# Performance work log

Measured on AMD Instinct MI355X. Metric: run time of the kernel, lower is better.

Reference implementation:

```python
import jax, jax.numpy as jnp
import numpy as np

B, L, H = 32, 512, 1024
H2 = H // 2          # split half = 512
D_ATTN = 64
EPS = 1e-5


def setup_inputs() -> dict:
    key = jax.random.key(0)
    ks = jax.random.split(key, 6)
    x = jax.random.normal(ks[0], (B, L, H), dtype=jnp.float32)
    # LayerNorm params (default torch init: weight=1, bias=0)
    ln_gamma = jnp.ones((H2,), jnp.float32)
    ln_beta = jnp.zeros((H2,), jnp.float32)
    # Toeplitz params (module inits w_vector=0, bias=1; use small random w for nontrivial math)
    w_vector = jax.random.normal(ks[1], (2 * L - 1,), jnp.float32) * 0.02
    t_bias = jnp.ones((L,), jnp.float32)
    # TinyAttention: kqv Linear(H2 -> 3*d_attn), proj Linear(d_attn -> H2)
    kqv_w = jax.random.normal(ks[2], (H2, 3 * D_ATTN), jnp.float32) * 0.02
    kqv_b = jnp.zeros((3 * D_ATTN,), jnp.float32)
    proj_w = jax.random.normal(ks[3], (D_ATTN, H2), jnp.float32) * 0.02
    proj_b = jnp.zeros((H2,), jnp.float32)
    return {"x": x, "ln_gamma": ln_gamma, "ln_beta": ln_beta,
            "w_vector": w_vector, "t_bias": t_bias,
            "kqv_w": kqv_w, "kqv_b": kqv_b, "proj_w": proj_w, "proj_b": proj_b}


def _toeplitz(w_vector):
    # Faithful replication of get_toeplitz(): pad, tile, trim, reshape, crop.
    r = w_vector.shape[0] // 2            # = L - 1
    t = jnp.pad(w_vector, (0, L))         # length 3L - 1
    t = jnp.tile(t, L)[:-L]               # length L * (3L - 2)
    t = t.reshape(L, 3 * L - 2)
    return t[:, r:-r]                      # [L, L]


def _tiny_attention(v, kqv_w, kqv_b, proj_w, proj_b):
    kqv = v @ kqv_w + kqv_b                        # [B, L, 3*d_attn]
    k, q, val = jnp.split(kqv, 3, axis=-1)         # chunk order: key, query, value
    scale = 1.0 / jnp.sqrt(jnp.float32(q.shape[-1]))
    scores = jnp.einsum('bqd,bkd->bqk', q, k) * scale
    soft = jax.nn.softmax(scores, axis=-1)
    head = jnp.einsum('bqk,bkd->bqd', soft, val)   # [B, L, d_attn]
    return head @ proj_w + proj_b                  # [B, L, H2]


def reference(x, ln_gamma, ln_beta, w_vector, t_bias, kqv_w, kqv_b, proj_w, proj_b):
    u, v = jnp.split(x, 2, axis=-1)                # each [B, L, H2]
    head = _tiny_attention(v, kqv_w, kqv_b, proj_w, proj_b)
    # LayerNorm over last dim
    mu = jnp.mean(v, axis=-1, keepdims=True)
    var = jnp.mean(jnp.square(v - mu), axis=-1, keepdims=True)
    vn = (v - mu) * jax.lax.rsqrt(var + EPS) * ln_gamma + ln_beta
    # spatial (Toeplitz) mixing: permute -> [B, H2, L], matmul [L, L], bias
    w_t = _toeplitz(w_vector)
    vm = jnp.einsum('blc,lm->bmc', vn, w_t.T).transpose(0, 2, 1)  # keep faithful: vp @ w_t
    vm = jnp.einsum('bcl,lm->bcm', vn.transpose(0, 2, 1), w_t) + t_bias
    v_out = vm.transpose(0, 2, 1) + head           # [B, L, H2]
    return u * v_out
```

## Files before the change

kernel.cpp:

```cpp
#include <hip/hip_runtime.h>
#include <math.h>

#define NB 32
#define LL 512
#define HH 1024
#define H2 512
#define DA 64

typedef unsigned int u32;
typedef unsigned short u16;
typedef __bf16 bf16x8 __attribute__((ext_vector_type(8)));
typedef float f32x4 __attribute__((ext_vector_type(4)));

__device__ __forceinline__ u16 f2bu(float f) {
    u32 u = __builtin_bit_cast(u32, f);
    u = (u + 0x7fff + ((u >> 16) & 1)) >> 16;
    return (u16)u;
}

__device__ __forceinline__ float b2f(u16 u) {
    u32 v = (u32)u << 16;
    return __builtin_bit_cast(float, v);
}

__device__ __forceinline__ void async_cp16(const void* g, void* l) {
    __builtin_amdgcn_global_load_lds(
        (const __attribute__((address_space(1))) u32*)g,
        (__attribute__((address_space(3))) u32*)l, 16, 0, 0);
}

__global__ void prep_kernel(const float* __restrict__ wv,
                            const float* __restrict__ kqvw,
                            const float* __restrict__ projw,
                            u16* __restrict__ wt, u16* __restrict__ kqvwT,
                            u16* __restrict__ projwT) {
    int e = blockIdx.x * 256 + threadIdx.x;
    if (e < 262144) {
        int m = e >> 9, l = e & 511;
        wt[e] = f2bu(wv[511 + m - l]);
    } else if (e < 262144 + 98304) {
        int i = e - 262144;
        int n = i >> 9, k = i & 511;
        kqvwT[i] = f2bu(kqvw[(size_t)k * 192 + n]);
    } else {
        int i = e - 360448;
        int c = i >> 6, d = i & 63;
        projwT[i] = f2bu(projw[(size_t)d * 512 + c]);
    }
}

__global__ __launch_bounds__(256, 2)
void front_kernel(const float* __restrict__ x,
                  const float* __restrict__ gamma, const float* __restrict__ beta,
                  const u16* __restrict__ kqvwT, const float* __restrict__ kqvb,
                  u16* __restrict__ vnT,
                  u16* __restrict__ qb, u16* __restrict__ kb, u16* __restrict__ vT) {
    __shared__ u16 Bs[2][192 * 32];
    __shared__ u16 T[512 * 34];
    __shared__ float MUs[32], RSs[32];
    int blk = blockIdx.x, t = threadIdx.x;
    int b = blk >> 4, l0 = (blk & 15) * 32;
    int lane = t & 63, wid = t >> 6;
    int l15 = lane & 15, q16 = lane >> 4, q8 = q16 * 8;

#pragma unroll
    for (int s = 0; s < 3; ++s) {
        int ci = t + s * 256;
        int grow = ci >> 2, gcol = ((ci & 3) ^ (grow & 3)) << 3;
        async_cp16(kqvwT + (size_t)grow * 512 + gcol, &Bs[0][ci * 8]);
    }

    int r = t >> 3, q = t & 7;
    const float* xr = x + ((size_t)(b * LL + l0 + r)) * HH + H2;
    float s1 = 0.0f, s2 = 0.0f;
#pragma unroll
    for (int i = 0; i < 16; ++i) {
        float4 v = *(const float4*)(xr + q * 64 + i * 4);
        s1 += v.x + v.y + v.z + v.w;
        s2 += v.x * v.x + v.y * v.y + v.z * v.z + v.w * v.w;
        int c = q * 64 + i * 4;
        T[(c + 0) * 34 + r] = f2bu(v.x);
        T[(c + 1) * 34 + r] = f2bu(v.y);
        T[(c + 2) * 34 + r] = f2bu(v.z);
        T[(c + 3) * 34 + r] = f2bu(v.w);
    }
    s1 += __shfl_xor(s1, 1); s2 += __shfl_xor(s2, 1);
    s1 += __shfl_xor(s1, 2); s2 += __shfl_xor(s2, 2);
    s1 += __shfl_xor(s1, 4); s2 += __shfl_xor(s2, 4);
    float mu = s1 * (1.0f / H2);
    float rstd = rsqrtf(s2 * (1.0f / H2) - mu * mu + 1e-5f);
    if ((t & 7) == 0) { MUs[r] = mu; RSs[r] = rstd; }
    __syncthreads();

    {
        int cc = t >> 2, seg = t & 3;
        float m0 = MUs[seg * 8 + 0], r0s = RSs[seg * 8 + 0];
        float m1 = MUs[seg * 8 + 1], r1s = RSs[seg * 8 + 1];
        float m2 = MUs[seg * 8 + 2], r2s = RSs[seg * 8 + 2];
        float m3 = MUs[seg * 8 + 3], r3s = RSs[seg * 8 + 3];
        float m4 = MUs[seg * 8 + 4], r4s = RSs[seg * 8 + 4];
        float m5 = MUs[seg * 8 + 5], r5s = RSs[seg * 8 + 5];
        float m6 = MUs[seg * 8 + 6], r6s = RSs[seg * 8 + 6];
        float m7 = MUs[seg * 8 + 7], r7s = RSs[seg * 8 + 7];
#pragma unroll
        for (int pass = 0; pass < 8; ++pass) {
            int c = pass * 64 + cc;
            float ga = gamma[c], be = beta[c];
            const u16* Tp = T + c * 34 + seg * 8;
            ushort4 t0 = ((const ushort4*)Tp)[0];
            ushort4 t1 = ((const ushort4*)Tp)[1];
            ushort4 o0, o1;
            o0.x = f2bu((b2f(t0.x) - m0) * r0s * ga + be);
            o0.y = f2bu((b2f(t0.y) - m1) * r1s * ga + be);
            o0.z = f2bu((b2f(t0.z) - m2) * r2s * ga + be);
            o0.w = f2bu((b2f(t0.w) - m3) * r3s * ga + be);
            o1.x = f2bu((b2f(t1.x) - m4) * r4s * ga + be);
            o1.y = f2bu((b2f(t1.y) - m5) * r5s * ga + be);
            o1.z = f2bu((b2f(t1.z) - m6) * r6s * ga + be);
            o1.w = f2bu((b2f(t1.w) - m7) * r7s * ga + be);
            u16* dst = vnT + ((size_t)(b * H2 + c)) * LL + l0 + seg * 8;
            ((ushort4*)dst)[0] = o0;
            ((ushort4*)dst)[1] = o1;
        }
    }

    int wm = (wid & 1) * 16, wn = (wid >> 1) * 96;
    int rowA = wm + l15;
    f32x4 acc[6] = {};
    for (int it = 0; it < 16; ++it) {
        if (it < 15) {
            int k0n = (it + 1) * 32, bfn = (it + 1) & 1;
#pragma unroll
            for (int s = 0; s < 3; ++s) {
                int ci = t + s * 256;
                int grow = ci >> 2, gcol = ((ci & 3) ^ (grow & 3)) << 3;
                async_cp16(kqvwT + (size_t)grow * 512 + k0n + gcol, &Bs[bfn][ci * 8]);
            }
        }
        bf16x8 a;
        int kb0 = it * 32 + q8;
#pragma unroll
        for (int u = 0; u < 8; ++u)
            a[u] = __builtin_bit_cast(__bf16, T[(kb0 + u) * 34 + rowA]);
        const u16* Bp = &Bs[it & 1][0];
#pragma unroll
        for (int j = 0; j < 6; ++j) {
            int n = wn + j * 16 + l15;
            bf16x8 bb = *(const bf16x8*)(Bp + (n * 4 + (q16 ^ (n & 3))) * 8);
            acc[j] = __builtin_amdgcn_mfma_f32_16x16x32_bf16(a, bb, acc[j], 0, 0, 0);
        }
        __syncthreads();
    }

    u16* Ts = &Bs[0][0];
    int rq = q16 * 4;
#pragma unroll
    for (int rr = 0; rr < 4; ++rr) {
        int mloc = wm + rq + rr;
        size_t mg = (size_t)(b * LL + l0 + mloc);
#pragma unroll
        for (int j = 0; j < 6; ++j) {
            int n = wn + j * 16 + l15;
            u16 hv = f2bu(acc[j][rr] + kqvb[n]);
            if (n < 64)       kb[mg * 64 + n] = hv;
            else if (n < 128) qb[mg * 64 + (n - 64)] = hv;
            else              Ts[(n - 128) * 36 + mloc] = hv;
        }
    }
    __syncthreads();
    int d = t >> 2, lo2 = (t & 3) * 8;
    u16* dst = vT + ((size_t)(b * 64 + d)) * 512 + l0 + lo2;
    const u16* src = Ts + d * 36 + lo2;
    ((ushort4*)dst)[0] = ((const ushort4*)src)[0];
    ((ushort4*)dst)[1] = ((const ushort4*)src)[1];
}

#define VLD 136
__global__ __launch_bounds__(256, 4)
void attn_kernel(const u16* __restrict__ qb, const u16* __restrict__ kb,
                 const u16* __restrict__ vT, u16* __restrict__ head) {
    __shared__ u16 Ps[4 * 16 * VLD];
    __shared__ float Osh[4][16 * 65];
    __shared__ float Msh[4][16], Lsh[4][16];
    int b = blockIdx.y, q0 = blockIdx.x * 16;
    int t = threadIdx.x, lane = t & 63, w = t >> 6;
    int l15 = lane & 15, q16 = lane >> 4, q8 = q16 * 8;
    int kc = w * 128;
    const u16* qg = qb + (size_t)b * LL * DA;
    const u16* kg = kb + (size_t)b * LL * DA;
    const u16* vg = vT + (size_t)b * DA * LL;

    bf16x8 aq[2];
#pragma unroll
    for (int s = 0; s < 2; ++s)
        aq[s] = *(const bf16x8*)(qg + (size_t)(q0 + l15) * DA + s * 32 + q8);

    f32x4 sc[8] = {};
#pragma unroll
    for (int j = 0; j < 8; ++j) {
#pragma unroll
        for (int s = 0; s < 2; ++s) {
            bf16x8 bk = *(const bf16x8*)(kg + (size_t)(kc + j * 16 + l15) * DA + s * 32 + q8);
            sc[j] = __builtin_amdgcn_mfma_f32_16x16x32_bf16(aq[s], bk, sc[j], 0, 0, 0);
        }
    }
    float mx[4], sm[4];
#pragma unroll
    for (int j = 0; j < 8; ++j)
#pragma unroll
        for (int rr = 0; rr < 4; ++rr) sc[j][rr] *= 0.125f;
#pragma unroll
    for (int rr = 0; rr < 4; ++rr) {
        float m0 = sc[0][rr];
#pragma unroll
        for (int j = 1; j < 8; ++j) m0 = fmaxf(m0, sc[j][rr]);
        m0 = fmaxf(m0, __shfl_xor(m0, 1));
        m0 = fmaxf(m0, __shfl_xor(m0, 2));
        m0 = fmaxf(m0, __shfl_xor(m0, 4));
        m0 = fmaxf(m0, __shfl_xor(m0, 8));
        mx[rr] = m0;
    }
#pragma unroll
    for (int j = 0; j < 8; ++j)
#pragma unroll
        for (int rr = 0; rr < 4; ++rr) sc[j][rr] = __expf(sc[j][rr] - mx[rr]);
#pragma unroll
    for (int rr = 0; rr < 4; ++rr) {
        float s0 = sc[0][rr];
#pragma unroll
        for (int j = 1; j < 8; ++j) s0 += sc[j][rr];
        s0 += __shfl_xor(s0, 1);
        s0 += __shfl_xor(s0, 2);
        s0 += __shfl_xor(s0, 4);
        s0 += __shfl_xor(s0, 8);
        sm[rr] = s0;
    }
    u16* Pw = Ps + w * 16 * VLD;
#pragma unroll
    for (int j = 0; j < 8; ++j)
#pragma unroll
        for (int rr = 0; rr < 4; ++rr)
            Pw[(q16 * 4 + rr) * VLD + j * 16 + l15] = f2bu(sc[j][rr]);
    f32x4 o[4] = {};
#pragma unroll
    for (int kt = 0; kt < 4; ++kt) {
        bf16x8 ap = *(const bf16x8*)(Pw + l15 * VLD + kt * 32 + q8);
#pragma unroll
        for (int j = 0; j < 4; ++j) {
            bf16x8 bv = *(const bf16x8*)(vg + (size_t)(j * 16 + l15) * LL + kc + kt * 32 + q8);
            o[j] = __builtin_amdgcn_mfma_f32_16x16x32_bf16(ap, bv, o[j], 0, 0, 0);
        }
    }
#pragma unroll
    for (int j = 0; j < 4; ++j)
#pragma unroll
        for (int rr = 0; rr < 4; ++rr)
            Osh[w][(q16 * 4 + rr) * 65 + j * 16 + l15] = o[j][rr];
    if (l15 == 0) {
#pragma unroll
        for (int rr = 0; rr < 4; ++rr) {
            Msh[w][q16 * 4 + rr] = mx[rr];
            Lsh[w][q16 * 4 + rr] = sm[rr];
        }
    }
    __syncthreads();
    int qq = t >> 4, dg = (t & 15) * 4;
    float m0 = Msh[0][qq], m1 = Msh[1][qq], m2 = Msh[2][qq], m3 = Msh[3][qq];
    float ms = fmaxf(fmaxf(m0, m1), fmaxf(m2, m3));
    float f0 = __expf(m0 - ms), f1 = __expf(m1 - ms), f2 = __expf(m2 - ms), f3 = __expf(m3 - ms);
    float lst = Lsh[0][qq] * f0 + Lsh[1][qq] * f1 + Lsh[2][qq] * f2 + Lsh[3][qq] * f3;
    float inv = 1.0f / lst;
    ushort4 res;
    u16* rp = (u16*)&res;
#pragma unroll
    for (int i = 0; i < 4; ++i) {
        int idx = qq * 65 + dg + i;
        float a = Osh[0][idx] * f0 + Osh[1][idx] * f1 + Osh[2][idx] * f2 + Osh[3][idx] * f3;
        rp[i] = f2bu(a * inv);
    }
    *(ushort4*)(head + (size_t)(b * LL + q0 + qq) * DA + dg) = res;
}

__device__ __forceinline__ void mfma_tile64(const u16* As, const u16* Bs,
                                            f32x4 acc[4][4], int wm, int wn,
                                            int l15, int q16) {
    int s7 = l15 & 7;
#pragma unroll
    for (int kk = 0; kk < 2; ++kk) {
        int j0 = kk * 4 + q16;
        bf16x8 a[4], bv[4];
#pragma unroll
        for (int i = 0; i < 4; ++i) {
            int row = wm + i * 16 + l15;
            a[i] = *(const bf16x8*)(As + (row * 8 + (j0 ^ s7)) * 8);
        }
#pragma unroll
        for (int j = 0; j < 4; ++j) {
            int row = wn + j * 16 + l15;
            bv[j] = *(const bf16x8*)(Bs + (row * 8 + (j0 ^ s7)) * 8);
        }
#pragma unroll
        for (int i = 0; i < 4; ++i)
#pragma unroll
            for (int j = 0; j < 4; ++j)
                acc[i][j] = __builtin_amdgcn_mfma_f32_16x16x32_bf16(a[i], bv[j], acc[i][j], 0, 0, 0);
    }
}

__device__ __forceinline__ void stage_pair(const u16* A, const u16* B, int ldk,
                                           int koff, u16* Ad, u16* Bd, int t) {
#pragma unroll
    for (int s = 0; s < 4; ++s) {
        int ci = t + s * 256;
        int grow = ci >> 3, gcol = ((ci & 7) ^ (grow & 7)) << 3;
        async_cp16(A + (size_t)grow * ldk + koff + gcol, Ad + ci * 8);
        async_cp16(B + (size_t)grow * ldk + koff + gcol, Bd + ci * 8);
    }
}

__global__ __launch_bounds__(256, 2)
void mix_kernel(const u16* __restrict__ wt,
                const u16* __restrict__ vnT,
                const u16* __restrict__ headb,
                const u16* __restrict__ projwT,
                const float* __restrict__ x,
                const float* __restrict__ tbias,
                const float* __restrict__ projb,
                float* __restrict__ out) {
    __shared__ u16 As[2][128 * 64];
    __shared__ u16 Bs[2][128 * 64];
    int lid = blockIdx.x;
    int p8 = lid & 7, rest = lid >> 3;
    int mi = rest & 3, pair = (rest >> 2) * 8 + p8;
    int b = pair >> 2, m0 = mi * 128, c0 = (pair & 3) * 128;
    int t = threadIdx.x, lane = t & 63, wid = t >> 6;
    int wm = (wid >> 1) * 64, wn = (wid & 1) * 64;
    int l15 = lane & 15, q16 = lane >> 4;
    f32x4 acc[4][4] = {};
    const u16* Ag = wt + (size_t)m0 * 512;
    const u16* Bg = vnT + ((size_t)b * H2 + c0) * 512;
    const u16* Hg = headb + ((size_t)b * LL + m0) * DA;
    const u16* Pg = projwT + (size_t)c0 * DA;

    stage_pair(Ag, Bg, 512, 0, As[0], Bs[0], t);
    __syncthreads();

    for (int it = 0; it < 9; ++it) {
        int nx = it + 1;
        if (nx < 8)
            stage_pair(Ag, Bg, 512, nx * 64, As[nx & 1], Bs[nx & 1], t);
        else if (nx == 8)
            stage_pair(Hg, Pg, 64, 0, As[0], Bs[0], t);
        mfma_tile64(As[it & 1], Bs[it & 1], acc, wm, wn, l15, q16);
        __syncthreads();
    }

    int rq = q16 * 4;
#pragma unroll
    for (int i = 0; i < 4; ++i) {
#pragma unroll
        for (int rr = 0; rr < 4; ++rr) {
            int m = m0 + wm + i * 16 + rq + rr;
            float tb = tbias[m];
            const float* xrow = x + ((size_t)b * LL + m) * HH;
            float* orow = out + ((size_t)b * LL + m) * H2;
#pragma unroll
            for (int j = 0; j < 4; ++j) {
                int c = c0 + wn + j * 16 + l15;
                float val = acc[i][j][rr] + tb + projb[c];
                orow[c] = xrow[c] * val;
            }
        }
    }
}

extern "C" void kernel_launch(void* const* d_in, const int* in_sizes, int n_in,
                              void* d_out, int out_size, void* d_ws, size_t ws_size,
                              hipStream_t stream) {
    (void)in_sizes; (void)n_in; (void)out_size; (void)ws_size;
    const float* x     = (const float*)d_in[0];
    const float* gamma = (const float*)d_in[1];
    const float* beta  = (const float*)d_in[2];
    const float* wv    = (const float*)d_in[3];
    const float* tb    = (const float*)d_in[4];
    const float* kqvw  = (const float*)d_in[5];
    const float* kqvb  = (const float*)d_in[6];
    const float* projw = (const float*)d_in[7];
    const float* projb = (const float*)d_in[8];
    float* out = (float*)d_out;

    u16* vnT_bf  = (u16*)d_ws;
    u16* qb      = vnT_bf + (size_t)NB * LL * H2;
    u16* kb      = qb + (size_t)NB * LL * DA;
    u16* vTb     = kb + (size_t)NB * LL * DA;
    u16* head_bf = vTb + (size_t)NB * LL * DA;
    u16* wt_bf   = head_bf + (size_t)NB * LL * DA;
    u16* kqvwT   = wt_bf + 512 * 512;
    u16* projwT  = kqvwT + 192 * 512;

    prep_kernel <<<1536, 256, 0, stream>>>(wv, kqvw, projw, wt_bf, kqvwT, projwT);
    front_kernel<<<512, 256, 0, stream>>>(x, gamma, beta, kqvwT, kqvb,
                                          vnT_bf, qb, kb, vTb);
    attn_kernel <<<dim3(32, NB), 256, 0, stream>>>(qb, kb, vTb, head_bf);
    mix_kernel  <<<512, 256, 0, stream>>>(wt_bf, vnT_bf, head_bf, projwT,
                                          x, tb, projb, out);
}
```

Baseline: 173.5 us.

## Precompute LayerNorm stats in prep kernel and shrink front kernel tiles

```diff
diff --git a/kernel.cpp b/kernel.cpp
--- a/kernel.cpp
+++ b/kernel.cpp
@@ -32,147 +32,137 @@
 __global__ void prep_kernel(const float* __restrict__ wv,
                             const float* __restrict__ kqvw,
                             const float* __restrict__ projw,
+                            const float* __restrict__ x,
                             u16* __restrict__ wt, u16* __restrict__ kqvwT,
-                            u16* __restrict__ projwT) {
-    int e = blockIdx.x * 256 + threadIdx.x;
-    if (e < 262144) {
-        int m = e >> 9, l = e & 511;
-        wt[e] = f2bu(wv[511 + m - l]);
-    } else if (e < 262144 + 98304) {
-        int i = e - 262144;
-        int n = i >> 9, k = i & 511;
-        kqvwT[i] = f2bu(kqvw[(size_t)k * 192 + n]);
+                            u16* __restrict__ projwT, float2* __restrict__ stats) {
+    int blk = blockIdx.x, t = threadIdx.x;
+    if (blk < 1536) {
+        int e = blk * 256 + t;
+        if (e < 262144) {
+            int m = e >> 9, l = e & 511;
+            wt[e] = f2bu(wv[511 + m - l]);
+        } else if (e < 262144 + 98304) {
+            int i = e - 262144;
+            int n = i >> 9, k = i & 511;
+            kqvwT[i] = f2bu(kqvw[(size_t)k * 192 + n]);
+        } else {
+            int i = e - 360448;
+            int c = i >> 6, d = i & 63;
+            projwT[i] = f2bu(projw[(size_t)d * 512 + c]);
+        }
     } else {
-        int i = e - 360448;
-        int c = i >> 6, d = i & 63;
-        projwT[i] = f2bu(projw[(size_t)d * 512 + c]);
-    }
-}
-
-__global__ __launch_bounds__(256, 2)
+        int row = (blk - 1536) * 4 + (t >> 6);
+        int lane = t & 63;
+        const float* xr = x + (size_t)row * HH + H2;
+        float4 a = *(const float4*)(xr + lane * 4);
+        float4 c = *(const float4*)(xr + 256 + lane * 4);
+        float s1 = a.x + a.y + a.z + a.w + c.x + c.y + c.z + c.w;
+        float s2 = a.x*a.x + a.y*a.y + a.z*a.z + a.w*a.w
+                 + c.x*c.x + c.y*c.y + c.z*c.z + c.w*c.w;
+        s1 += __shfl_xor(s1, 1);  s2 += __shfl_xor(s2, 1);
+        s1 += __shfl_xor(s1, 2);  s2 += __shfl_xor(s2, 2);
+        s1 += __shfl_xor(s1, 4);  s2 += __shfl_xor(s2, 4);
+        s1 += __shfl_xor(s1, 8);  s2 += __shfl_xor(s2, 8);
+        s1 += __shfl_xor(s1, 16); s2 += __shfl_xor(s2, 16);
+        s1 += __shfl_xor(s1, 32); s2 += __shfl_xor(s2, 32);
+        if (lane == 0) {
+            float mu = s1 * (1.0f / H2);
+            float rstd = rsqrtf(s2 * (1.0f / H2) - mu * mu + 1e-5f);
+            stats[row] = make_float2(mu, rstd);
+        }
+    }
+}
+
+__global__ __launch_bounds__(256, 4)
 void front_kernel(const float* __restrict__ x,
                   const float* __restrict__ gamma, const float* __restrict__ beta,
+                  const float2* __restrict__ stats,
                   const u16* __restrict__ kqvwT, const float* __restrict__ kqvb,
                   u16* __restrict__ vnT,
                   u16* __restrict__ qb, u16* __restrict__ kb, u16* __restrict__ vT) {
-    __shared__ u16 Bs[2][192 * 32];
-    __shared__ u16 T[512 * 34];
-    __shared__ float MUs[32], RSs[32];
+    __shared__ u16 T[512 * 18];
     int blk = blockIdx.x, t = threadIdx.x;
-    int b = blk >> 4, l0 = (blk & 15) * 32;
+    int b = blk >> 5, l0 = (blk & 31) * 16;
     int lane = t & 63, wid = t >> 6;
     int l15 = lane & 15, q16 = lane >> 4, q8 = q16 * 8;
 
-#pragma unroll
-    for (int s = 0; s < 3; ++s) {
-        int ci = t + s * 256;
-        int grow = ci >> 2, gcol = ((ci & 3) ^ (grow & 3)) << 3;
-        async_cp16(kqvwT + (size_t)grow * 512 + gcol, &Bs[0][ci * 8]);
-    }
-
-    int r = t >> 3, q = t & 7;
-    const float* xr = x + ((size_t)(b * LL + l0 + r)) * HH + H2;
-    float s1 = 0.0f, s2 = 0.0f;
-#pragma unroll
-    for (int i = 0; i < 16; ++i) {
-        float4 v = *(const float4*)(xr + q * 64 + i * 4);
-        s1 += v.x + v.y + v.z + v.w;
-        s2 += v.x * v.x + v.y * v.y + v.z * v.z + v.w * v.w;
-        int c = q * 64 + i * 4;
-        T[(c + 0) * 34 + r] = f2bu(v.x);
-        T[(c + 1) * 34 + r] = f2bu(v.y);
-        T[(c + 2) * 34 + r] = f2bu(v.z);
-        T[(c + 3) * 34 + r] = f2bu(v.w);
-    }
-    s1 += __shfl_xor(s1, 1); s2 += __shfl_xor(s2, 1);
-    s1 += __shfl_xor(s1, 2); s2 += __shfl_xor(s2, 2);
-    s1 += __shfl_xor(s1, 4); s2 += __shfl_xor(s2, 4);
-    float mu = s1 * (1.0f / H2);
-    float rstd = rsqrtf(s2 * (1.0f / H2) - mu * mu + 1e-5f);
-    if ((t & 7) == 0) { MUs[r] = mu; RSs[r] = rstd; }
-    __syncthreads();
-
     {
-        int cc = t >> 2, seg = t & 3;
-        float m0 = MUs[seg * 8 + 0], r0s = RSs[seg * 8 + 0];
-        float m1 = MUs[seg * 8 + 1], r1s = RSs[seg * 8 + 1];
-        float m2 = MUs[seg * 8 + 2], r2s = RSs[seg * 8 + 2];
-        float m3 = MUs[seg * 8 + 3], r3s = RSs[seg * 8 + 3];
-        float m4 = MUs[seg * 8 + 4], r4s = RSs[seg * 8 + 4];
-        float m5 = MUs[seg * 8 + 5], r5s = RSs[seg * 8 + 5];
-        float m6 = MUs[seg * 8 + 6], r6s = RSs[seg * 8 + 6];
-        float m7 = MUs[seg * 8 + 7], r7s = RSs[seg * 8 + 7];
-#pragma unroll
-        for (int pass = 0; pass < 8; ++pass) {
-            int c = pass * 64 + cc;
-            float ga = gamma[c], be = beta[c];
-            const u16* Tp = T + c * 34 + seg * 8;
+        int r = t >> 4;
+        int c00 = (t & 15) * 4;
+        float2 st = stats[(size_t)(b * LL + l0 + r)];
+        const float* xr = x + ((size_t)(b * LL + l0 + r)) * HH + H2;
+#pragma unroll
+        for (int i = 0; i < 8; ++i) {
+            int c = c00 + i * 64;
+            float4 v = *(const float4*)(xr + c);
+            float4 g = *(const float4*)(gamma + c);
+            float4 be = *(const float4*)(beta + c);
+            T[(c + 0) * 18 + r] = f2bu((v.x - st.x) * st.y * g.x + be.x);
+            T[(c + 1) * 18 + r] = f2bu((v.y - st.x) * st.y * g.y + be.y);
+            T[(c + 2) * 18 + r] = f2bu((v.z - st.x) * st.y * g.z + be.z);
+            T[(c + 3) * 18 + r] = f2bu((v.w - st.x) * st.y * g.w + be.w);
+        }
+    }
+    __syncthreads();
+
+    {
+        int cb = t >> 1, h = t & 1;
+#pragma unroll
+        for (int pass = 0; pass < 4; ++pass) {
+            int c = pass * 128 + cb;
+            const u16* Tp = T + c * 18 + h * 8;
             ushort4 t0 = ((const ushort4*)Tp)[0];
-            ushort4 t1 = ((const ushort4*)Tp)[1];
-            ushort4 o0, o1;
-            o0.x = f2bu((b2f(t0.x) - m0) * r0s * ga + be);
-            o0.y = f2bu((b2f(t0.y) - m1) * r1s * ga + be);
-            o0.z = f2bu((b2f(t0.z) - m2) * r2s * ga + be);
-            o0.w = f2bu((b2f(t0.w) - m3) * r3s * ga + be);
-            o1.x = f2bu((b2f(t1.x) - m4) * r4s * ga + be);
-            o1.y = f2bu((b2f(t1.y) - m5) * r5s * ga + be);
-            o1.z = f2bu((b2f(t1.z) - m6) * r6s * ga + be);
-            o1.w = f2bu((b2f(t1.w) - m7) * r7s * ga + be);
-            u16* dst = vnT + ((size_t)(b * H2 + c)) * LL + l0 + seg * 8;
-            ((ushort4*)dst)[0] = o0;
-            ((ushort4*)dst)[1] = o1;
-        }
-    }
-
-    int wm = (wid & 1) * 16, wn = (wid >> 1) * 96;
-    int rowA = wm + l15;
-    f32x4 acc[6] = {};
+            ushort4 t1 = ((const ushort4*)(Tp + 4))[0];
+            u16* dst = vnT + ((size_t)(b * H2 + c)) * LL + l0 + h * 8;
+            ((ushort4*)dst)[0] = t0;
+            ((ushort4*)dst)[1] = t1;
+        }
+    }
+
+    int wn = wid * 48;
+    size_t arow = ((size_t)(b * LL + l0 + l15)) * HH + H2;
+    f32x4 acc[3] = {};
+#pragma unroll 4
     for (int it = 0; it < 16; ++it) {
-        if (it < 15) {
-            int k0n = (it + 1) * 32, bfn = (it + 1) & 1;
-#pragma unroll
-            for (int s = 0; s < 3; ++s) {
-                int ci = t + s * 256;
-                int grow = ci >> 2, gcol = ((ci & 3) ^ (grow & 3)) << 3;
-                async_cp16(kqvwT + (size_t)grow * 512 + k0n + gcol, &Bs[bfn][ci * 8]);
-            }
-        }
+        float4 v0 = *(const float4*)(x + arow + it * 32 + q8);
+        float4 v1 = *(const float4*)(x + arow + it * 32 + q8 + 4);
         bf16x8 a;
-        int kb0 = it * 32 + q8;
-#pragma unroll
-        for (int u = 0; u < 8; ++u)
-            a[u] = __builtin_bit_cast(__bf16, T[(kb0 + u) * 34 + rowA]);
-        const u16* Bp = &Bs[it & 1][0];
-#pragma unroll
-        for (int j = 0; j < 6; ++j) {
-            int n = wn + j * 16 + l15;
-            bf16x8 bb = *(const bf16x8*)(Bp + (n * 4 + (q16 ^ (n & 3))) * 8);
+        a[0] = __builtin_bit_cast(__bf16, f2bu(v0.x));
+        a[1] = __builtin_bit_cast(__bf16, f2bu(v0.y));
+        a[2] = __builtin_bit_cast(__bf16, f2bu(v0.z));
+        a[3] = __builtin_bit_cast(__bf16, f2bu(v0.w));
+        a[4] = __builtin_bit_cast(__bf16, f2bu(v1.x));
+        a[5] = __builtin_bit_cast(__bf16, f2bu(v1.y));
+        a[6] = __builtin_bit_cast(__bf16, f2bu(v1.z));
+        a[7] = __builtin_bit_cast(__bf16, f2bu(v1.w));
+        const u16* Bb = kqvwT + it * 32 + q8;
+#pragma unroll
+        for (int j = 0; j < 3; ++j) {
+            bf16x8 bb = *(const bf16x8*)(Bb + (size_t)(wn + j * 16 + l15) * 512);
             acc[j] = __builtin_amdgcn_mfma_f32_16x16x32_bf16(a, bb, acc[j], 0, 0, 0);
         }
-        __syncthreads();
-    }
-
-    u16* Ts = &Bs[0][0];
+    }
+
+    __syncthreads();
+    u16* Ts = T;
     int rq = q16 * 4;
 #pragma unroll
     for (int rr = 0; rr < 4; ++rr) {
-        int mloc = wm + rq + rr;
+        int mloc = rq + rr;
         size_t mg = (size_t)(b * LL + l0 + mloc);
 #pragma unroll
-        for (int j = 0; j < 6; ++j) {
+        for (int j = 0; j < 3; ++j) {
             int n = wn + j * 16 + l15;
             u16 hv = f2bu(acc[j][rr] + kqvb[n]);
             if (n < 64)       kb[mg * 64 + n] = hv;
             else if (n < 128) qb[mg * 64 + (n - 64)] = hv;
-            else              Ts[(n - 128) * 36 + mloc] = hv;
-        }
-    }
-    __syncthreads();
-    int d = t >> 2, lo2 = (t & 3) * 8;
-    u16* dst = vT + ((size_t)(b * 64 + d)) * 512 + l0 + lo2;
-    const u16* src = Ts + d * 36 + lo2;
-    ((ushort4*)dst)[0] = ((const ushort4*)src)[0];
-    ((ushort4*)dst)[1] = ((const ushort4*)src)[1];
+            else              Ts[(n - 128) * 20 + mloc] = hv;
+        }
+    }
+    __syncthreads();
+    int d = t >> 2, lo2 = (t & 3) * 4;
+    *(ushort4*)(vT + ((size_t)(b * 64 + d)) * 512 + l0 + lo2) =
+        *(const ushort4*)(Ts + d * 20 + lo2);
 }
 
 #define VLD 136
@@ -397,10 +387,12 @@
     u16* wt_bf   = head_bf + (size_t)NB * LL * DA;
     u16* kqvwT   = wt_bf + 512 * 512;
     u16* projwT  = kqvwT + 192 * 512;
-
-    prep_kernel <<<1536, 256, 0, stream>>>(wv, kqvw, projw, wt_bf, kqvwT, projwT);
-    front_kernel<<<512, 256, 0, stream>>>(x, gamma, beta, kqvwT, kqvb,
-                                          vnT_bf, qb, kb, vTb);
+    float2* stats = (float2*)(projwT + 64 * 512);
+
+    prep_kernel <<<5632, 256, 0, stream>>>(wv, kqvw, projw, x, wt_bf, kqvwT,
+                                           projwT, stats);
+    front_kernel<<<1024, 256, 0, stream>>>(x, gamma, beta, stats, kqvwT, kqvb,
+                                           vnT_bf, qb, kb, vTb);
     attn_kernel <<<dim3(32, NB), 256, 0, stream>>>(qb, kb, vTb, head_bf);
     mix_kernel  <<<512, 256, 0, stream>>>(wt_bf, vnT_bf, head_bf, projwT,
                                           x, tb, projb, out);
```

After: 199.8 us. +15.1%, slower.

## Split LayerNorm-transpose and KQV projection into separate kernels

Applied to the files above, without the earlier changes.

```diff
diff --git a/kernel.cpp b/kernel.cpp
--- a/kernel.cpp
+++ b/kernel.cpp
@@ -49,130 +49,141 @@
     }
 }
 
-__global__ __launch_bounds__(256, 2)
+__global__ __launch_bounds__(512, 4)
 void front_kernel(const float* __restrict__ x,
                   const float* __restrict__ gamma, const float* __restrict__ beta,
-                  const u16* __restrict__ kqvwT, const float* __restrict__ kqvb,
-                  u16* __restrict__ vnT,
-                  u16* __restrict__ qb, u16* __restrict__ kb, u16* __restrict__ vT) {
-    __shared__ u16 Bs[2][192 * 32];
-    __shared__ u16 T[512 * 34];
-    __shared__ float MUs[32], RSs[32];
+                  u16* __restrict__ vnT) {
+    __shared__ u16 T[512 * 36];
     int blk = blockIdx.x, t = threadIdx.x;
     int b = blk >> 4, l0 = (blk & 15) * 32;
-    int lane = t & 63, wid = t >> 6;
-    int l15 = lane & 15, q16 = lane >> 4, q8 = q16 * 8;
-
-#pragma unroll
-    for (int s = 0; s < 3; ++s) {
-        int ci = t + s * 256;
-        int grow = ci >> 2, gcol = ((ci & 3) ^ (grow & 3)) << 3;
-        async_cp16(kqvwT + (size_t)grow * 512 + gcol, &Bs[0][ci * 8]);
-    }
-
-    int r = t >> 3, q = t & 7;
+    int r = t >> 4, cl = t & 15;
+    int rs = r ^ ((cl & 3) << 3);
     const float* xr = x + ((size_t)(b * LL + l0 + r)) * HH + H2;
+
+    float4 v[8];
+#pragma unroll
+    for (int i = 0; i < 8; ++i) v[i] = *(const float4*)(xr + i * 64 + cl * 4);
     float s1 = 0.0f, s2 = 0.0f;
 #pragma unroll
-    for (int i = 0; i < 16; ++i) {
-        float4 v = *(const float4*)(xr + q * 64 + i * 4);
-        s1 += v.x + v.y + v.z + v.w;
-        s2 += v.x * v.x + v.y * v.y + v.z * v.z + v.w * v.w;
-        int c = q * 64 + i * 4;
-        T[(c + 0) * 34 + r] = f2bu(v.x);
-        T[(c + 1) * 34 + r] = f2bu(v.y);
-        T[(c + 2) * 34 + r] = f2bu(v.z);
-        T[(c + 3) * 34 + r] = f2bu(v.w);
+    for (int i = 0; i < 8; ++i) {
+        s1 += v[i].x + v[i].y + v[i].z + v[i].w;
+        s2 += v[i].x * v[i].x + v[i].y * v[i].y + v[i].z * v[i].z + v[i].w * v[i].w;
     }
     s1 += __shfl_xor(s1, 1); s2 += __shfl_xor(s2, 1);
     s1 += __shfl_xor(s1, 2); s2 += __shfl_xor(s2, 2);
     s1 += __shfl_xor(s1, 4); s2 += __shfl_xor(s2, 4);
+    s1 += __shfl_xor(s1, 8); s2 += __shfl_xor(s2, 8);
     float mu = s1 * (1.0f / H2);
     float rstd = rsqrtf(s2 * (1.0f / H2) - mu * mu + 1e-5f);
-    if ((t & 7) == 0) { MUs[r] = mu; RSs[r] = rstd; }
+
+#pragma unroll
+    for (int hh = 0; hh < 2; ++hh) {
+        float4 g[4], be[4];
+#pragma unroll
+        for (int i = 0; i < 4; ++i) {
+            g[i]  = *(const float4*)(gamma + (hh * 4 + i) * 64 + cl * 4);
+            be[i] = *(const float4*)(beta  + (hh * 4 + i) * 64 + cl * 4);
+        }
+#pragma unroll
+        for (int i = 0; i < 4; ++i) {
+            int ii = hh * 4 + i;
+            int c = ii * 64 + cl * 4;
+            float4 vv = v[ii];
+            T[(c + 0) * 36 + rs] = f2bu((vv.x - mu) * rstd * g[i].x + be[i].x);
+            T[(c + 1) * 36 + rs] = f2bu((vv.y - mu) * rstd * g[i].y + be[i].y);
+            T[(c + 2) * 36 + rs] = f2bu((vv.z - mu) * rstd * g[i].z + be[i].z);
+            T[(c + 3) * 36 + rs] = f2bu((vv.w - mu) * rstd * g[i].w + be[i].w);
+        }
+    }
     __syncthreads();
 
+    int c = t;
+    int swzB = ((c >> 2) & 3) << 3;
+    const u16* Tp = T + c * 36;
+    ushort4 o[8];
+#pragma unroll
+    for (int h = 0; h < 8; ++h)
+        o[h] = *(const ushort4*)(Tp + ((h << 2) ^ swzB));
+    u16* dst = vnT + ((size_t)(b * H2 + c)) * LL + l0;
+#pragma unroll
+    for (int h = 0; h < 4; ++h) {
+        union { ushort4 u2[2]; uint4 q; } pk;
+        pk.u2[0] = o[2 * h]; pk.u2[1] = o[2 * h + 1];
+        ((uint4*)dst)[h] = pk.q;
+    }
+}
+
+__global__ __launch_bounds__(256, 4)
+void kqv_kernel(const float* __restrict__ x,
+                const u16* __restrict__ kqvwT, const float* __restrict__ kqvb,
+                u16* __restrict__ qb, u16* __restrict__ kb, u16* __restrict__ vT) {
+    __shared__ u16 Ks[16 * 64];
+    __shared__ u16 Qs[16 * 64];
+    __shared__ u16 Vs[64 * 40];
+    int blk = blockIdx.x, t = threadIdx.x;
+    int R0 = blk * 16;
+    int b = R0 >> 9, l0 = R0 & 511;
+    int lane = t & 63, wid = t >> 6;
+    int l15 = lane & 15, q16 = lane >> 4, q8 = q16 * 8;
+    int n0 = wid * 48;
+    const float* xa = x + ((size_t)(R0 + l15)) * HH + H2;
+    const u16* Bb = kqvwT + (size_t)(n0 + l15) * 512;
+
+    f32x4 acc[3] = {};
+    float4 a0 = *(const float4*)(xa + q8);
+    float4 a1 = *(const float4*)(xa + q8 + 4);
+    bf16x8 b0 = *(const bf16x8*)(Bb + 0 * 8192 + q8);
+    bf16x8 b1 = *(const bf16x8*)(Bb + 1 * 8192 + q8);
+    bf16x8 b2 = *(const bf16x8*)(Bb + 2 * 8192 + q8);
+#pragma unroll
+    for (int it = 0; it < 16; ++it) {
+        float4 na0, na1; bf16x8 nb0, nb1, nb2;
+        if (it < 15) {
+            int ko = (it + 1) * 32 + q8;
+            na0 = *(const float4*)(xa + ko);
+            na1 = *(const float4*)(xa + ko + 4);
+            nb0 = *(const bf16x8*)(Bb + 0 * 8192 + ko);
+            nb1 = *(const bf16x8*)(Bb + 1 * 8192 + ko);
+            nb2 = *(const bf16x8*)(Bb + 2 * 8192 + ko);
+        }
+        bf16x8 a;
+        a[0] = __builtin_bit_cast(__bf16, f2bu(a0.x));
+        a[1] = __builtin_bit_cast(__bf16, f2bu(a0.y));
+        a[2] = __builtin_bit_cast(__bf16, f2bu(a0.z));
+        a[3] = __builtin_bit_cast(__bf16, f2bu(a0.w));
+        a[4] = __builtin_bit_cast(__bf16, f2bu(a1.x));
+        a[5] = __builtin_bit_cast(__bf16, f2bu(a1.y));
+        a[6] = __builtin_bit_cast(__bf16, f2bu(a1.z));
+        a[7] = __builtin_bit_cast(__bf16, f2bu(a1.w));
+        acc[0] = __builtin_amdgcn_mfma_f32_16x16x32_bf16(a, b0, acc[0], 0, 0, 0);
+        acc[1] = __builtin_amdgcn_mfma_f32_16x16x32_bf16(a, b1, acc[1], 0, 0, 0);
+        acc[2] = __builtin_amdgcn_mfma_f32_16x16x32_bf16(a, b2, acc[2], 0, 0, 0);
+        a0 = na0; a1 = na1; b0 = nb0; b1 = nb1; b2 = nb2;
+    }
+
+    int rq = q16 * 4;
+#pragma unroll
+    for (int j = 0; j < 3; ++j) {
+        int n = n0 + j * 16 + l15;
+        float bias = kqvb[n];
+#pragma unroll
+        for (int rr = 0; rr < 4; ++rr) {
+            int m = rq + rr;
+            u16 hv = f2bu(acc[j][rr] + bias);
+            if (n < 64)       Ks[m * 64 + n] = hv;
+            else if (n < 128) Qs[m * 64 + (n - 64)] = hv;
+            else              Vs[(n - 128) * 40 + m] = hv;
+        }
+    }
+    __syncthreads();
     {
-        int cc = t >> 2, seg = t & 3;
-        float m0 = MUs[seg * 8 + 0], r0s = RSs[seg * 8 + 0];
-        float m1 = MUs[seg * 8 + 1], r1s = RSs[seg * 8 + 1];
-        float m2 = MUs[seg * 8 + 2], r2s = RSs[seg * 8 + 2];
-        float m3 = MUs[seg * 8 + 3], r3s = RSs[seg * 8 + 3];
-        float m4 = MUs[seg * 8 + 4], r4s = RSs[seg * 8 + 4];
-        float m5 = MUs[seg * 8 + 5], r5s = RSs[seg * 8 + 5];
-        float m6 = MUs[seg * 8 + 6], r6s = RSs[seg * 8 + 6];
-        float m7 = MUs[seg * 8 + 7], r7s = RSs[seg * 8 + 7];
-#pragma unroll
-        for (int pass = 0; pass < 8; ++pass) {
-            int c = pass * 64 + cc;
-            float ga = gamma[c], be = beta[c];
-            const u16* Tp = T + c * 34 + seg * 8;
-            ushort4 t0 = ((const ushort4*)Tp)[0];
-            ushort4 t1 = ((const ushort4*)Tp)[1];
-            ushort4 o0, o1;
-            o0.x = f2bu((b2f(t0.x) - m0) * r0s * ga + be);
-            o0.y = f2bu((b2f(t0.y) - m1) * r1s * ga + be);
-            o0.z = f2bu((b2f(t0.z) - m2) * r2s * ga + be);
-            o0.w = f2bu((b2f(t0.w) - m3) * r3s * ga + be);
-            o1.x = f2bu((b2f(t1.x) - m4) * r4s * ga + be);
-            o1.y = f2bu((b2f(t1.y) - m5) * r5s * ga + be);
-            o1.z = f2bu((b2f(t1.z) - m6) * r6s * ga + be);
-            o1.w = f2bu((b2f(t1.w) - m7) * r7s * ga + be);
-            u16* dst = vnT + ((size_t)(b * H2 + c)) * LL + l0 + seg * 8;
-            ((ushort4*)dst)[0] = o0;
-            ((ushort4*)dst)[1] = o1;
-        }
-    }
-
-    int wm = (wid & 1) * 16, wn = (wid >> 1) * 96;
-    int rowA = wm + l15;
-    f32x4 acc[6] = {};
-    for (int it = 0; it < 16; ++it) {
-        if (it < 15) {
-            int k0n = (it + 1) * 32, bfn = (it + 1) & 1;
-#pragma unroll
-            for (int s = 0; s < 3; ++s) {
-                int ci = t + s * 256;
-                int grow = ci >> 2, gcol = ((ci & 3) ^ (grow & 3)) << 3;
-                async_cp16(kqvwT + (size_t)grow * 512 + k0n + gcol, &Bs[bfn][ci * 8]);
-            }
-        }
-        bf16x8 a;
-        int kb0 = it * 32 + q8;
-#pragma unroll
-        for (int u = 0; u < 8; ++u)
-            a[u] = __builtin_bit_cast(__bf16, T[(kb0 + u) * 34 + rowA]);
-        const u16* Bp = &Bs[it & 1][0];
-#pragma unroll
-        for (int j = 0; j < 6; ++j) {
-            int n = wn + j * 16 + l15;
-            bf16x8 bb = *(const bf16x8*)(Bp + (n * 4 + (q16 ^ (n & 3))) * 8);
-            acc[j] = __builtin_amdgcn_mfma_f32_16x16x32_bf16(a, bb, acc[j], 0, 0, 0);
-        }
-        __syncthreads();
-    }
-
-    u16* Ts = &Bs[0][0];
-    int rq = q16 * 4;
-#pragma unroll
-    for (int rr = 0; rr < 4; ++rr) {
-        int mloc = wm + rq + rr;
-        size_t mg = (size_t)(b * LL + l0 + mloc);
-#pragma unroll
-        for (int j = 0; j < 6; ++j) {
-            int n = wn + j * 16 + l15;
-            u16 hv = f2bu(acc[j][rr] + kqvb[n]);
-            if (n < 64)       kb[mg * 64 + n] = hv;
-            else if (n < 128) qb[mg * 64 + (n - 64)] = hv;
-            else              Ts[(n - 128) * 36 + mloc] = hv;
-        }
-    }
-    __syncthreads();
-    int d = t >> 2, lo2 = (t & 3) * 8;
-    u16* dst = vT + ((size_t)(b * 64 + d)) * 512 + l0 + lo2;
-    const u16* src = Ts + d * 36 + lo2;
-    ((ushort4*)dst)[0] = ((const ushort4*)src)[0];
-    ((ushort4*)dst)[1] = ((const ushort4*)src)[1];
+        size_t base = (size_t)R0 * 64;
+        *(ushort4*)(kb + base + t * 4) = *(const ushort4*)(Ks + t * 4);
+        *(ushort4*)(qb + base + t * 4) = *(const ushort4*)(Qs + t * 4);
+        int d = t >> 2, ls = (t & 3) * 4;
+        *(ushort4*)(vT + ((size_t)(b * 64 + d)) * 512 + l0 + ls) =
+            *(const ushort4*)(Vs + d * 40 + ls);
+    }
 }
 
 #define VLD 136
@@ -399,8 +410,8 @@
     u16* projwT  = kqvwT + 192 * 512;
 
     prep_kernel <<<1536, 256, 0, stream>>>(wv, kqvw, projw, wt_bf, kqvwT, projwT);
-    front_kernel<<<512, 256, 0, stream>>>(x, gamma, beta, kqvwT, kqvb,
-                                          vnT_bf, qb, kb, vTb);
+    front_kernel<<<512, 512, 0, stream>>>(x, gamma, beta, vnT_bf);
+    kqv_kernel  <<<1024, 256, 0, stream>>>(x, kqvwT, kqvb, qb, kb, vTb);
     attn_kernel <<<dim3(32, NB), 256, 0, stream>>>(qb, kb, vTb, head_bf);
     mix_kernel  <<<512, 256, 0, stream>>>(wt_bf, vnT_bf, head_bf, projwT,
                                           x, tb, projb, out);
```

Measured after the change: 201.7 us. 1.16x slower.
